# Optimization experiments

Measured on AMD Instinct MI355X. Metric: run time of the kernel, lower is better.

Reference implementation:

```python
import jax, jax.numpy as jnp
import numpy as np

KSIZE = 3


def _windows(img, ksize):
    # img: [B, 1, H, W] -> [B, 1, H, W, ksize*ksize] sliding windows with reflect pad
    p = ksize // 2
    padded = jnp.pad(img, ((0, 0), (0, 0), (p, p), (p, p)), mode='reflect')
    H, W = img.shape[2], img.shape[3]
    wins = [padded[:, :, i:i + H, j:j + W] for i in range(ksize) for j in range(ksize)]
    return jnp.stack(wins, axis=-1)


def setup_inputs() -> dict:
    key = jax.random.key(0)
    x = jax.random.normal(key, (8, 3, 512, 512), dtype=jnp.float32)
    return {"x": x}


def reference(x):
    ksize = KSIZE
    center_idx = x.shape[1] // 2
    center = x[:, center_idx:center_idx + 1]            # [B,1,H,W]
    wins = _windows(center, ksize)                      # [B,1,H,W,k*k]
    med = jnp.median(wins, axis=-1)                     # local median (odd k*k -> exact element)
    mad = jnp.median(jnp.abs(wins - med[..., None]), axis=-1)  # median abs deviation
    return mad
```

## Files before the change

kernel.cpp:

```cpp
#include <hip/hip_runtime.h>
#include <hip/hip_bf16.h>

#define CMPSWAP(a, b) { float _t = fminf(a, b); (b) = fmaxf(a, b); (a) = _t; }

__device__ __forceinline__ float median9(float p0, float p1, float p2,
                                         float p3, float p4, float p5,
                                         float p6, float p7, float p8) {
    CMPSWAP(p1, p2); CMPSWAP(p4, p5); CMPSWAP(p7, p8);
    CMPSWAP(p0, p1); CMPSWAP(p3, p4); CMPSWAP(p6, p7);
    CMPSWAP(p1, p2); CMPSWAP(p4, p5); CMPSWAP(p7, p8);
    CMPSWAP(p0, p3); CMPSWAP(p5, p8); CMPSWAP(p4, p7);
    CMPSWAP(p3, p6); CMPSWAP(p1, p4); CMPSWAP(p2, p5);
    CMPSWAP(p4, p7); CMPSWAP(p4, p2); CMPSWAP(p6, p4);
    CMPSWAP(p4, p2);
    return p4;
}

__device__ __forceinline__ float mad9(float v0, float v1, float v2,
                                      float v3, float v4, float v5,
                                      float v6, float v7, float v8) {
    float med = median9(v0, v1, v2, v3, v4, v5, v6, v7, v8);
    return median9(fabsf(v0 - med), fabsf(v1 - med), fabsf(v2 - med),
                   fabsf(v3 - med), fabsf(v4 - med), fabsf(v5 - med),
                   fabsf(v6 - med), fabsf(v7 - med), fabsf(v8 - med));
}

__global__ void __launch_bounds__(256)
mad_kernel(const float* __restrict__ x, float* __restrict__ out) {
    const int W = 512;
    int idx = blockIdx.x * blockDim.x + threadIdx.x;
    int g  = idx & 127;
    int py = (idx >> 7) & 511;
    int b  = idx >> 16;
    int px0 = g << 2;

    const float* base = x + ((size_t)(b * 3 + 1)) * (512 * 512);

    int ym = (py == 0)   ? 1   : py - 1;
    int yp = (py == 511) ? 510 : py + 1;

    const float* r0 = base + ym * W;
    const float* r1 = base + py * W;
    const float* r2 = base + yp * W;

    int xl = (px0 == 0)   ? 1   : px0 - 1;
    int xr = (px0 == 508) ? 510 : px0 + 4;

    float4 c0 = *reinterpret_cast<const float4*>(r0 + px0);
    float4 c1 = *reinterpret_cast<const float4*>(r1 + px0);
    float4 c2 = *reinterpret_cast<const float4*>(r2 + px0);
    float l0 = r0[xl], l1 = r1[xl], l2 = r2[xl];
    float q0 = r0[xr], q1 = r1[xr], q2 = r2[xr];

    float4 o;
    o.x = mad9(l0,   c0.x, c0.y,  l1,   c1.x, c1.y,  l2,   c2.x, c2.y);
    o.y = mad9(c0.x, c0.y, c0.z,  c1.x, c1.y, c1.z,  c2.x, c2.y, c2.z);
    o.z = mad9(c0.y, c0.z, c0.w,  c1.y, c1.z, c1.w,  c2.y, c2.z, c2.w);
    o.w = mad9(c0.z, c0.w, q0,    c1.z, c1.w, q1,    c2.z, c2.w, q2);

    *reinterpret_cast<float4*>(out + ((size_t)idx << 2)) = o;
}

extern "C" void kernel_launch(void* const* d_in, const int* in_sizes, int n_in,
                              void* d_out, int out_size, void* d_ws, size_t ws_size,
                              hipStream_t stream) {
    const float* x = (const float*)d_in[0];
    float* out = (float*)d_out;
    const int groups = 8 * 512 * 128;
    const int block = 256;
    const int grid = groups / block;
    mad_kernel<<<grid, block, 0, stream>>>(x, out);
}
```

Before: 11.56 us.

## Share sorted column triples and merge networks across four pixels, closed-form MAD

Each 3-element column is sorted once, and adjacent column pairs are merged into shared sorted 6-lists that neighbouring pixels reuse. Each pixel then merges one 6-list with one 3-column into a fully sorted 9-list. The MAD is computed in closed form from that sorted window as the 5th smallest absolute deviation, using min/max pairs instead of a second median network. This cuts the compare-swap count per pixel, trading it for more live registers. The kernel is likely memory-bound at this size, so less ALU work may matter little.

```diff
diff --git a/kernel.cpp b/kernel.cpp
--- a/kernel.cpp
+++ b/kernel.cpp
@@ -1,28 +1,65 @@
 #include <hip/hip_runtime.h>
 #include <hip/hip_bf16.h>
 
-#define CMPSWAP(a, b) { float _t = fminf(a, b); (b) = fmaxf(a, b); (a) = _t; }
-
-__device__ __forceinline__ float median9(float p0, float p1, float p2,
-                                         float p3, float p4, float p5,
-                                         float p6, float p7, float p8) {
-    CMPSWAP(p1, p2); CMPSWAP(p4, p5); CMPSWAP(p7, p8);
-    CMPSWAP(p0, p1); CMPSWAP(p3, p4); CMPSWAP(p6, p7);
-    CMPSWAP(p1, p2); CMPSWAP(p4, p5); CMPSWAP(p7, p8);
-    CMPSWAP(p0, p3); CMPSWAP(p5, p8); CMPSWAP(p4, p7);
-    CMPSWAP(p3, p6); CMPSWAP(p1, p4); CMPSWAP(p2, p5);
-    CMPSWAP(p4, p7); CMPSWAP(p4, p2); CMPSWAP(p6, p4);
-    CMPSWAP(p4, p2);
-    return p4;
+__device__ __forceinline__ void ce(float& a, float& b) {
+    float t = fminf(a, b); b = fmaxf(a, b); a = t;
+}
+__device__ __forceinline__ void s3(float& a, float& b, float& c) {
+    ce(a, b); ce(a, c); ce(b, c);
 }
 
-__device__ __forceinline__ float mad9(float v0, float v1, float v2,
-                                      float v3, float v4, float v5,
-                                      float v6, float v7, float v8) {
-    float med = median9(v0, v1, v2, v3, v4, v5, v6, v7, v8);
-    return median9(fabsf(v0 - med), fabsf(v1 - med), fabsf(v2 - med),
-                   fabsf(v3 - med), fabsf(v4 - med), fabsf(v5 - med),
-                   fabsf(v6 - med), fabsf(v7 - med), fabsf(v8 - med));
+__device__ __forceinline__ void merge21(float x0, float x1, float y0,
+                                        float& p0, float& p1, float& p2) {
+    ce(x0, y0);
+    p0 = x0; p1 = y0; p2 = x1; ce(p1, p2);
+}
+
+__device__ __forceinline__ void merge33(float a0, float a1, float a2,
+                                        float b0, float b1, float b2,
+                                        float& w0, float& w1, float& w2,
+                                        float& w3, float& w4, float& w5) {
+    float x0 = a0, x1 = a2, y0 = b0, y1 = b2;
+    ce(x0, y0); ce(x1, y1); ce(x1, y0);
+    float e0 = a1, e1 = b1; ce(e0, e1);
+    w0 = x0;
+    w1 = x1; w2 = e0; ce(w1, w2);
+    w3 = y0; w4 = e1; ce(w3, w4);
+    w5 = y1;
+}
+
+__device__ __forceinline__ void merge63(float c0, float c1, float c2, float c3, float c4, float c5,
+                                        float d0, float d1, float d2,
+                                        float& w0, float& w1, float& w2, float& w3, float& w4,
+                                        float& w5, float& w6, float& w7, float& w8) {
+    float p0, p1, p2; merge21(c0, c4, d0, p0, p1, p2);
+    float q0 = c2, q1 = d2; ce(q0, q1);
+    float o0 = p0, o1 = p1, o2 = q0; ce(o1, o2);
+    float o3 = p2, o4 = q1; ce(o3, o4);
+    float r0, r1, r2; merge21(c1, c5, d1, r0, r1, r2);
+    float e0 = r0, e1 = r1, e2 = c3; ce(e1, e2);
+    float e3 = r2;
+    w0 = o0;
+    w1 = o1; w2 = e0; ce(w1, w2);
+    w3 = o2; w4 = e1; ce(w3, w4);
+    w5 = o3; w6 = e2; ce(w5, w6);
+    w7 = o4; w8 = e3; ce(w7, w8);
+}
+
+__device__ __forceinline__ float mad_sorted9(float w0, float w1, float w2, float w3, float w4,
+                                             float w5, float w6, float w7, float w8) {
+    float m = w4;
+    float m0 = fminf(m - w3, w8 - m);
+    float m1 = fminf(m - w2, w7 - m);
+    float m2 = fminf(m - w1, w6 - m);
+    float m3 = fminf(m - w0, w5 - m);
+    return fmaxf(fmaxf(m0, m1), fmaxf(m2, m3));
+}
+
+__device__ __forceinline__ float mad_px(float c0, float c1, float c2, float c3, float c4, float c5,
+                                        float d0, float d1, float d2) {
+    float w0, w1, w2, w3, w4, w5, w6, w7, w8;
+    merge63(c0, c1, c2, c3, c4, c5, d0, d1, d2, w0, w1, w2, w3, w4, w5, w6, w7, w8);
+    return mad_sorted9(w0, w1, w2, w3, w4, w5, w6, w7, w8);
 }
 
 __global__ void __launch_bounds__(256)
@@ -52,11 +89,25 @@
     float l0 = r0[xl], l1 = r1[xl], l2 = r2[xl];
     float q0 = r0[xr], q1 = r1[xr], q2 = r2[xr];
 
+    float A0 = l0,   A1 = l1,   A2 = l2;   s3(A0, A1, A2);
+    float B0 = c0.x, B1 = c1.x, B2 = c2.x; s3(B0, B1, B2);
+    float C0 = c0.y, C1 = c1.y, C2 = c2.y; s3(C0, C1, C2);
+    float D0 = c0.z, D1 = c1.z, D2 = c2.z; s3(D0, D1, D2);
+    float E0 = c0.w, E1 = c1.w, E2 = c2.w; s3(E0, E1, E2);
+    float F0 = q0,   F1 = q1,   F2 = q2;   s3(F0, F1, F2);
+
+    float M01_0, M01_1, M01_2, M01_3, M01_4, M01_5;
+    merge33(A0, A1, A2, B0, B1, B2, M01_0, M01_1, M01_2, M01_3, M01_4, M01_5);
+    float M23_0, M23_1, M23_2, M23_3, M23_4, M23_5;
+    merge33(C0, C1, C2, D0, D1, D2, M23_0, M23_1, M23_2, M23_3, M23_4, M23_5);
+    float M45_0, M45_1, M45_2, M45_3, M45_4, M45_5;
+    merge33(E0, E1, E2, F0, F1, F2, M45_0, M45_1, M45_2, M45_3, M45_4, M45_5);
+
     float4 o;
-    o.x = mad9(l0,   c0.x, c0.y,  l1,   c1.x, c1.y,  l2,   c2.x, c2.y);
-    o.y = mad9(c0.x, c0.y, c0.z,  c1.x, c1.y, c1.z,  c2.x, c2.y, c2.z);
-    o.z = mad9(c0.y, c0.z, c0.w,  c1.y, c1.z, c1.w,  c2.y, c2.z, c2.w);
-    o.w = mad9(c0.z, c0.w, q0,    c1.z, c1.w, q1,    c2.z, c2.w, q2);
+    o.x = mad_px(M01_0, M01_1, M01_2, M01_3, M01_4, M01_5, C0, C1, C2);
+    o.y = mad_px(M23_0, M23_1, M23_2, M23_3, M23_4, M23_5, B0, B1, B2);
+    o.z = mad_px(M23_0, M23_1, M23_2, M23_3, M23_4, M23_5, E0, E1, E2);
+    o.w = mad_px(M45_0, M45_1, M45_2, M45_3, M45_4, M45_5, D0, D1, D2);
 
     *reinterpret_cast<float4*>(out + ((size_t)idx << 2)) = o;
 }
```

Measured after the change: 11.42 us. Within noise of the previous version (-1.1%).
